# Optimization experiments

Measured on AMD Instinct MI355X. Metric: run time of the kernel, lower is better.

The kernel has to match this reference:

```python
import jax, jax.numpy as jnp
import numpy as np

B, S, D_IN = 4, 2048, 1024
H, D_HEAD = 16, 64  # num_head, num_out; H*D_HEAD == D_IN here
LN_EPS = 1e-5


def setup_inputs() -> dict:
    key = jax.random.key(0)
    ks = jax.random.split(key, 5)
    scale = 1.0 / np.sqrt(D_IN)
    return {
        "x": jax.random.normal(ks[0], (B, S, D_IN), dtype=jnp.float32),
        "Wq": jax.random.normal(ks[1], (H * D_HEAD, D_IN), dtype=jnp.float32) * scale,
        "Wk": jax.random.normal(ks[2], (H * D_HEAD, D_IN), dtype=jnp.float32) * scale,
        "Wv": jax.random.normal(ks[3], (H * D_HEAD, D_IN), dtype=jnp.float32) * scale,
        "Wr": jax.random.normal(ks[4], (H * D_HEAD, D_IN), dtype=jnp.float32) * scale,
        "gamma": jnp.ones((H * D_HEAD,), dtype=jnp.float32),
        "beta": jnp.zeros((H * D_HEAD,), dtype=jnp.float32),
    }


def reference(x, Wq, Wk, Wv, Wr, gamma, beta):
    b, s, _ = x.shape
    # Linear (no bias), torch weight layout [out, in]; split heads head-major
    q = (x @ Wq.T).reshape(b, s, H, D_HEAD)
    k = (x @ Wk.T).reshape(b, s, H, D_HEAD)
    v = (x @ Wv.T).reshape(b, s, H, D_HEAD)
    # full O(S^2) score matrix, as in the original
    scores = jnp.einsum("bqhd,bkhd->bhqk", q, k) / jnp.sqrt(jnp.float32(D_HEAD))
    weights = jax.nn.softmax(scores, axis=-1)
    attn = jnp.einsum("bhqk,bkhd->bqhd", weights, v).reshape(b, s, H * D_HEAD)
    out = jax.nn.relu(attn + x @ Wr.T)
    # LayerNorm over last dim with affine params
    mu = jnp.mean(out, axis=-1, keepdims=True)
    var = jnp.mean(jnp.square(out - mu), axis=-1, keepdims=True)
    out = (out - mu) * jax.lax.rsqrt(var + LN_EPS) * gamma + beta
    return out
```

## Files before the change

kernel.cpp:

```cpp
#include <hip/hip_runtime.h>
#include <hip/hip_bf16.h>
#include <stdint.h>

constexpr int BB = 4;
constexpr int SS = 2048;
constexpr int DIN = 1024;
constexpr int HH = 16;
constexpr int DH = 64;
constexpr int NOUT = 4096;
constexpr int MROWS = BB * SS;

typedef __attribute__((ext_vector_type(8))) short bf16x8;
typedef __attribute__((ext_vector_type(8))) unsigned short u16x8;
typedef __attribute__((ext_vector_type(4))) unsigned short u16x4;
typedef __attribute__((ext_vector_type(4))) float f32x4;

__device__ __forceinline__ unsigned short f2bf(float f) {
  unsigned int x = __float_as_uint(f);
  unsigned int r = (x + 0x7fffu + ((x >> 16) & 1u)) >> 16;
  return (unsigned short)r;
}
__device__ __forceinline__ float bf2f(unsigned short u) {
  return __uint_as_float(((unsigned int)u) << 16);
}

__device__ __forceinline__ void gload16(const void* g, void* l) {
  typedef __attribute__((address_space(1))) void gvoid;
  typedef __attribute__((address_space(3))) void lvoid;
  __builtin_amdgcn_global_load_lds((gvoid*)(uintptr_t)g, (lvoid*)l, 16, 0, 0);
}

__global__ __launch_bounds__(256) void convert_x(const float* __restrict__ src,
                                                 unsigned short* __restrict__ dst) {
  int i = (blockIdx.x * 256 + threadIdx.x) * 8;
  f32x4 a = *(const f32x4*)(src + i);
  f32x4 b = *(const f32x4*)(src + i + 4);
  u16x8 o;
  o[0] = f2bf(a[0]); o[1] = f2bf(a[1]); o[2] = f2bf(a[2]); o[3] = f2bf(a[3]);
  o[4] = f2bf(b[0]); o[5] = f2bf(b[1]); o[6] = f2bf(b[2]); o[7] = f2bf(b[3]);
  *(u16x8*)(dst + i) = o;
}

__global__ __launch_bounds__(256) void convert_w(const float* __restrict__ Wq,
                                                 const float* __restrict__ Wk,
                                                 const float* __restrict__ Wv,
                                                 const float* __restrict__ Wr,
                                                 unsigned short* __restrict__ dst) {
  int i = (blockIdx.x * 256 + threadIdx.x) * 8;
  int seg = i >> 20;
  const float* src = (seg == 0) ? Wq : (seg == 1) ? Wk : (seg == 2) ? Wv : Wr;
  float scale = (seg == 0) ? 0.125f * 1.44269504088896f : 1.0f;
  int j = i & 1048575;
  f32x4 a = *(const f32x4*)(src + j);
  f32x4 b = *(const f32x4*)(src + j + 4);
  u16x8 o;
  o[0] = f2bf(a[0] * scale); o[1] = f2bf(a[1] * scale);
  o[2] = f2bf(a[2] * scale); o[3] = f2bf(a[3] * scale);
  o[4] = f2bf(b[0] * scale); o[5] = f2bf(b[1] * scale);
  o[6] = f2bf(b[2] * scale); o[7] = f2bf(b[3] * scale);
  *(u16x8*)(dst + i) = o;
}

constexpr int Bb_M = 128, Bb_N = 128, Bb_K = 32;

__global__ __launch_bounds__(256) void gemm_qkvr(const unsigned short* __restrict__ X,
                                                 const unsigned short* __restrict__ Wt,
                                                 unsigned short* __restrict__ Y) {
  const int K = DIN;
  const int nbn = NOUT / Bb_N;
  int bid = blockIdx.x;
  int idx = (bid & 7) * 256 + (bid >> 3);
  int bm = idx / nbn, bn = idx % nbn;
  int m0 = bm * Bb_M, n0 = bn * Bb_N;
  int t = threadIdx.x;
  int w = t >> 6, l = t & 63;
  int lg = l >> 4, ll = l & 15;
  int wm = (w >> 1) * 64, wn = (w & 1) * 64;

  __shared__ unsigned short As[Bb_M * Bb_K];
  __shared__ unsigned short Bs[Bb_N * Bb_K];

  f32x4 acc[4][4];
#pragma unroll
  for (int i = 0; i < 4; i++)
#pragma unroll
    for (int j = 0; j < 4; j++) acc[i][j] = (f32x4)0.0f;

  for (int k0 = 0; k0 < K; k0 += Bb_K) {
    __syncthreads();
#pragma unroll
    for (int it = 0; it < 2; ++it) {
      int c = w * 2 + it;
      int row = c * 16 + (l >> 2);
      int col = (l & 3) * 8;
      gload16(X + (size_t)(m0 + row) * K + k0 + col, &As[c * 512]);
      gload16(Wt + (size_t)(n0 + row) * K + k0 + col, &Bs[c * 512]);
    }
    __syncthreads();
    bf16x8 a[4], b[4];
#pragma unroll
    for (int mt = 0; mt < 4; ++mt)
      a[mt] = *(const bf16x8*)&As[(wm + mt * 16 + ll) * Bb_K + lg * 8];
#pragma unroll
    for (int nt = 0; nt < 4; ++nt)
      b[nt] = *(const bf16x8*)&Bs[(wn + nt * 16 + ll) * Bb_K + lg * 8];
#pragma unroll
    for (int mt = 0; mt < 4; ++mt)
#pragma unroll
      for (int nt = 0; nt < 4; ++nt)
        acc[mt][nt] = __builtin_amdgcn_mfma_f32_16x16x32_bf16(a[mt], b[nt], acc[mt][nt], 0, 0, 0);
  }
#pragma unroll
  for (int mt = 0; mt < 4; ++mt)
#pragma unroll
    for (int nt = 0; nt < 4; ++nt) {
      int n = n0 + wn + nt * 16 + ll;
#pragma unroll
      for (int r = 0; r < 4; ++r) {
        int m = m0 + wm + mt * 16 + lg * 4 + r;
        Y[(size_t)m * NOUT + n] = f2bf(acc[mt][nt][r]);
      }
    }
}

__global__ __launch_bounds__(256) void transpose_v(const unsigned short* __restrict__ qkvr,
                                                   unsigned short* __restrict__ vt) {
  int bh = blockIdx.x >> 5;
  int st = blockIdx.x & 31;
  int b = bh >> 4, h = bh & 15;
  __shared__ unsigned short tile[64][72];
  int t = threadIdx.x;
#pragma unroll
  for (int c = 0; c < 2; ++c) {
    int chunk = t + c * 256;
    int row = chunk >> 3;
    int col = (chunk & 7) * 8;
    u16x8 v = *(const u16x8*)(qkvr + (size_t)(b * SS + st * 64 + row) * NOUT + 2048 + h * DH + col);
    *(u16x8*)&tile[row][col] = v;
  }
  __syncthreads();
  int d = t >> 2;
  int s0 = (t & 3) * 16;
  u16x8 o0, o1;
#pragma unroll
  for (int i = 0; i < 8; ++i) o0[i] = tile[s0 + i][d];
#pragma unroll
  for (int i = 0; i < 8; ++i) o1[i] = tile[s0 + 8 + i][d];
  size_t orow = (size_t)(bh * DH + d) * SS + st * 64 + s0;
  *(u16x8*)(vt + orow) = o0;
  *(u16x8*)(vt + orow + 8) = o1;
}

__global__ __launch_bounds__(512) void attention(const unsigned short* __restrict__ qkvr,
                                                 const unsigned short* __restrict__ vt,
                                                 unsigned short* __restrict__ attn) {
  int bid = blockIdx.x;
  int idx = (bid & 7) * 64 + (bid >> 3);
  int qt = idx & 7;
  int bh = idx >> 3;
  int b = bh >> 4, h = bh & 15;
  int t = threadIdx.x, w = t >> 6, l = t & 63;
  int lg = l >> 4, ll = l & 15;

  __shared__ unsigned short Ks[2][4096];
  __shared__ unsigned short Vs[2][4096];
  __shared__ unsigned short Ps[8][2048];

  const unsigned short* kbase = qkvr + (size_t)(b * SS) * NOUT + 1024 + h * DH;
  const unsigned short* vbase = vt + (size_t)(bh * DH) * SS;

  bf16x8 qb[2][2];
#pragma unroll
  for (int m = 0; m < 2; ++m) {
    int qrow = b * SS + qt * 256 + w * 32 + m * 16 + ll;
#pragma unroll
    for (int kk = 0; kk < 2; ++kk)
      qb[m][kk] = *(const bf16x8*)(qkvr + (size_t)qrow * NOUT + h * DH + kk * 32 + lg * 8);
  }

  f32x4 acc[2][4];
#pragma unroll
  for (int m = 0; m < 2; ++m)
#pragma unroll
    for (int i = 0; i < 4; i++) acc[m][i] = (f32x4)0.0f;
  float lsum[2] = {0.0f, 0.0f};

  int grow = t >> 3;
  int gcol = ((t & 7) ^ (grow & 7)) * 8;

  auto stage = [&](int tile, int bi) {
    gload16(kbase + (size_t)(tile * 64 + grow) * NOUT + gcol, &Ks[bi][w * 512]);
    gload16(vbase + (size_t)grow * SS + tile * 64 + gcol, &Vs[bi][w * 512]);
  };

  stage(0, 0);

  for (int kt = 0; kt < 32; ++kt) {
    int bi = kt & 1;
    stage((kt + 1) & 31, bi ^ 1);
    asm volatile("s_waitcnt vmcnt(2)" ::: "memory");
    __builtin_amdgcn_s_barrier();
    __builtin_amdgcn_sched_barrier(0);

    f32x4 s[2][4];
#pragma unroll
    for (int m = 0; m < 2; ++m)
#pragma unroll
      for (int nt = 0; nt < 4; nt++) s[m][nt] = (f32x4)0.0f;
    __builtin_amdgcn_s_setprio(1);
#pragma unroll
    for (int nt = 0; nt < 4; ++nt)
#pragma unroll
      for (int kk = 0; kk < 2; ++kk) {
        bf16x8 kb = *(const bf16x8*)&Ks[bi][(nt * 16 + ll) * 64 + ((kk * 4 + lg) ^ (ll & 7)) * 8];
        s[0][nt] = __builtin_amdgcn_mfma_f32_16x16x32_bf16(kb, qb[0][kk], s[0][nt], 0, 0, 0);
        s[1][nt] = __builtin_amdgcn_mfma_f32_16x16x32_bf16(kb, qb[1][kk], s[1][nt], 0, 0, 0);
      }
    __builtin_amdgcn_s_setprio(0);

#pragma unroll
    for (int m = 0; m < 2; ++m) {
      float ps = 0.0f;
#pragma unroll
      for (int nt = 0; nt < 4; nt++)
#pragma unroll
        for (int r = 0; r < 4; r++) {
          float e;
          asm("v_exp_f32 %0, %1" : "=v"(e) : "v"(s[m][nt][r]));
          s[m][nt][r] = e;
          ps += e;
        }
      lsum[m] += ps;
    }

#pragma unroll
    for (int m = 0; m < 2; ++m) {
      char* prow = (char*)&Ps[w][0] + (m * 16 + ll) * 128;
#pragma unroll
      for (int nt = 0; nt < 4; nt++) {
        unsigned sp0, sp1;
        asm("v_cvt_pk_bf16_f32 %0, %1, %2" : "=v"(sp0) : "v"(s[m][nt][0]), "v"(s[m][nt][1]));
        asm("v_cvt_pk_bf16_f32 %0, %1, %2" : "=v"(sp1) : "v"(s[m][nt][2]), "v"(s[m][nt][3]));
        uint2 pv; pv.x = sp0; pv.y = sp1;
        *(uint2*)(prow + ((2 * nt + (lg >> 1)) ^ (ll & 7)) * 16 + (lg & 1) * 8) = pv;
      }
    }

    bf16x8 pa[2][2];
#pragma unroll
    for (int m = 0; m < 2; ++m)
#pragma unroll
      for (int kk = 0; kk < 2; ++kk)
        pa[m][kk] = *(const bf16x8*)((char*)&Ps[w][0] + (m * 16 + ll) * 128 +
                                     ((4 * kk + lg) ^ (ll & 7)) * 16);

    __builtin_amdgcn_s_setprio(1);
#pragma unroll
    for (int kk = 0; kk < 2; ++kk) {
#pragma unroll
      for (int dt = 0; dt < 4; ++dt) {
        bf16x8 vb = *(const bf16x8*)&Vs[bi][(dt * 16 + ll) * 64 + ((kk * 4 + lg) ^ (ll & 7)) * 8];
        acc[0][dt] = __builtin_amdgcn_mfma_f32_16x16x32_bf16(pa[0][kk], vb, acc[0][dt], 0, 0, 0);
        acc[1][dt] = __builtin_amdgcn_mfma_f32_16x16x32_bf16(pa[1][kk], vb, acc[1][dt], 0, 0, 0);
      }
    }
    __builtin_amdgcn_s_setprio(0);
    __builtin_amdgcn_s_barrier();
    __builtin_amdgcn_sched_barrier(0);
  }
  asm volatile("s_waitcnt vmcnt(0)" ::: "memory");

  float inv[2][4];
#pragma unroll
  for (int m = 0; m < 2; ++m) {
    float lr = lsum[m];
    lr += __shfl_xor(lr, 16);
    lr += __shfl_xor(lr, 32);
#pragma unroll
    for (int r = 0; r < 4; r++)
      inv[m][r] = 1.0f / __shfl(lr, lg * 4 + r);
  }
#pragma unroll
  for (int m = 0; m < 2; ++m)
#pragma unroll
    for (int r = 0; r < 4; r++) {
      int arow = b * SS + qt * 256 + w * 32 + m * 16 + lg * 4 + r;
#pragma unroll
      for (int dt = 0; dt < 4; dt++)
        attn[(size_t)arow * DIN + h * DH + dt * 16 + ll] = f2bf(acc[m][dt][r] * inv[m][r]);
    }
}

__global__ __launch_bounds__(256) void ln_epilogue(const unsigned short* __restrict__ attn,
                                                   const unsigned short* __restrict__ qkvr,
                                                   const float* __restrict__ gamma,
                                                   const float* __restrict__ beta,
                                                   float* __restrict__ out) {
  int row = blockIdx.x;
  int t = threadIdx.x;
  u16x4 av = *(const u16x4*)(attn + (size_t)row * DIN + t * 4);
  u16x4 rv = *(const u16x4*)(qkvr + (size_t)row * NOUT + 3072 + t * 4);
  float v[4];
  float s = 0.0f, s2 = 0.0f;
#pragma unroll
  for (int i = 0; i < 4; i++) {
    v[i] = fmaxf(bf2f(av[i]) + bf2f(rv[i]), 0.0f);
    s += v[i];
    s2 += v[i] * v[i];
  }
#pragma unroll
  for (int m = 1; m < 64; m <<= 1) {
    s += __shfl_xor(s, m);
    s2 += __shfl_xor(s2, m);
  }
  __shared__ float red[2][4];
  int w = t >> 6, l = t & 63;
  if (l == 0) { red[0][w] = s; red[1][w] = s2; }
  __syncthreads();
  s = red[0][0] + red[0][1] + red[0][2] + red[0][3];
  s2 = red[1][0] + red[1][1] + red[1][2] + red[1][3];
  float mu = s * (1.0f / 1024.0f);
  float var = s2 * (1.0f / 1024.0f) - mu * mu;
  float rstd = rsqrtf(var + 1e-5f);
  f32x4 g = *(const f32x4*)(gamma + t * 4);
  f32x4 be = *(const f32x4*)(beta + t * 4);
  f32x4 o;
#pragma unroll
  for (int i = 0; i < 4; i++) o[i] = (v[i] - mu) * rstd * g[i] + be[i];
  *(f32x4*)(out + (size_t)row * DIN + t * 4) = o;
}

extern "C" void kernel_launch(void* const* d_in, const int* in_sizes, int n_in,
                              void* d_out, int out_size, void* d_ws, size_t ws_size,
                              hipStream_t stream) {
  const float* x = (const float*)d_in[0];
  const float* Wq = (const float*)d_in[1];
  const float* Wk = (const float*)d_in[2];
  const float* Wv = (const float*)d_in[3];
  const float* Wr = (const float*)d_in[4];
  const float* gamma = (const float*)d_in[5];
  const float* beta = (const float*)d_in[6];
  float* out = (float*)d_out;

  char* ws = (char*)d_ws;
  unsigned short* x_bf = (unsigned short*)ws;
  unsigned short* w_bf = (unsigned short*)(ws + (16ull << 20));
  unsigned short* qkvr = (unsigned short*)(ws + (24ull << 20));
  unsigned short* vt   = (unsigned short*)(ws + (88ull << 20));
  unsigned short* attn = (unsigned short*)(ws + (104ull << 20));

  convert_x<<<4096, 256, 0, stream>>>(x, x_bf);
  convert_w<<<2048, 256, 0, stream>>>(Wq, Wk, Wv, Wr, w_bf);
  gemm_qkvr<<<(MROWS / Bb_M) * (NOUT / Bb_N), 256, 0, stream>>>(x_bf, w_bf, qkvr);
  transpose_v<<<2048, 256, 0, stream>>>(qkvr, vt);
  attention<<<512, 512, 0, stream>>>(qkvr, vt, attn);
  ln_epilogue<<<MROWS, 256, 0, stream>>>(attn, qkvr, gamma, beta, out);
}
```

Baseline: 196.4 us.

## Double-buffer QKVR GEMM with async LDS loads, XOR swizzle and BK=64

Rewrites the projection GEMM main loop to use two LDS buffers, each with a K-tile of 64. The loop prefetches the tile two steps ahead while MFMAs run on the current tile, and synchronises with explicit waitcnt and barriers instead of two __syncthreads per step. An XOR swizzle on the column slot is meant to cut LDS bank conflicts on fragment reads. LDS use grows to 64KB per block, which may limit occupancy. The wrapped prefetch on the final iterations issues redundant loads.

```diff
diff --git a/kernel.cpp b/kernel.cpp
--- a/kernel.cpp
+++ b/kernel.cpp
@@ -61,24 +61,24 @@
   *(u16x8*)(dst + i) = o;
 }
 
-constexpr int Bb_M = 128, Bb_N = 128, Bb_K = 32;
+constexpr int GBM = 128, GBN = 128, GBK = 64;
 
 __global__ __launch_bounds__(256) void gemm_qkvr(const unsigned short* __restrict__ X,
                                                  const unsigned short* __restrict__ Wt,
                                                  unsigned short* __restrict__ Y) {
   const int K = DIN;
-  const int nbn = NOUT / Bb_N;
+  const int nbn = NOUT / GBN;
   int bid = blockIdx.x;
   int idx = (bid & 7) * 256 + (bid >> 3);
   int bm = idx / nbn, bn = idx % nbn;
-  int m0 = bm * Bb_M, n0 = bn * Bb_N;
+  int m0 = bm * GBM, n0 = bn * GBN;
   int t = threadIdx.x;
   int w = t >> 6, l = t & 63;
   int lg = l >> 4, ll = l & 15;
   int wm = (w >> 1) * 64, wn = (w & 1) * 64;
 
-  __shared__ unsigned short As[Bb_M * Bb_K];
-  __shared__ unsigned short Bs[Bb_N * Bb_K];
+  __shared__ unsigned short As[2][GBM * GBK];
+  __shared__ unsigned short Bs[2][GBN * GBK];
 
   f32x4 acc[4][4];
 #pragma unroll
@@ -86,30 +86,64 @@
 #pragma unroll
     for (int j = 0; j < 4; j++) acc[i][j] = (f32x4)0.0f;
 
-  for (int k0 = 0; k0 < K; k0 += Bb_K) {
-    __syncthreads();
-#pragma unroll
-    for (int it = 0; it < 2; ++it) {
-      int c = w * 2 + it;
-      int row = c * 16 + (l >> 2);
-      int col = (l & 3) * 8;
-      gload16(X + (size_t)(m0 + row) * K + k0 + col, &As[c * 512]);
-      gload16(Wt + (size_t)(n0 + row) * K + k0 + col, &Bs[c * 512]);
-    }
-    __syncthreads();
-    bf16x8 a[4], b[4];
+  int grow = t >> 3;
+  int gslot = t & 7;
+
+  auto stage = [&](int kt, int bi) {
+    int k0 = kt * GBK;
+#pragma unroll
+    for (int c = 0; c < 4; ++c) {
+      int row = c * 32 + grow;
+      int col = (gslot ^ (row & 7)) * 8;
+      gload16(X + (size_t)(m0 + row) * K + k0 + col, &As[bi][c * 2048 + w * 512]);
+      gload16(Wt + (size_t)(n0 + row) * K + k0 + col, &Bs[bi][c * 2048 + w * 512]);
+    }
+  };
+
+  stage(0, 0);
+  stage(1, 1);
+  asm volatile("s_waitcnt vmcnt(8)" ::: "memory");
+  __builtin_amdgcn_s_barrier();
+  __builtin_amdgcn_sched_barrier(0);
+
+  for (int kt = 0; kt < 16; ++kt) {
+    int cur = kt & 1;
+    bf16x8 af[4][2], bfr[4][2];
 #pragma unroll
     for (int mt = 0; mt < 4; ++mt)
-      a[mt] = *(const bf16x8*)&As[(wm + mt * 16 + ll) * Bb_K + lg * 8];
+#pragma unroll
+      for (int kk = 0; kk < 2; ++kk)
+        af[mt][kk] = *(const bf16x8*)&As[cur][(wm + mt * 16 + ll) * GBK +
+                                             ((kk * 4 + lg) ^ (ll & 7)) * 8];
 #pragma unroll
     for (int nt = 0; nt < 4; ++nt)
-      b[nt] = *(const bf16x8*)&Bs[(wn + nt * 16 + ll) * Bb_K + lg * 8];
+#pragma unroll
+      for (int kk = 0; kk < 2; ++kk)
+        bfr[nt][kk] = *(const bf16x8*)&Bs[cur][(wn + nt * 16 + ll) * GBK +
+                                              ((kk * 4 + lg) ^ (ll & 7)) * 8];
+    asm volatile("s_waitcnt lgkmcnt(0)" ::: "memory");
+    __builtin_amdgcn_s_barrier();
+    __builtin_amdgcn_sched_barrier(0);
+
+    stage((kt + 2) & 15, cur);
+
+    __builtin_amdgcn_s_setprio(1);
 #pragma unroll
     for (int mt = 0; mt < 4; ++mt)
 #pragma unroll
       for (int nt = 0; nt < 4; ++nt)
-        acc[mt][nt] = __builtin_amdgcn_mfma_f32_16x16x32_bf16(a[mt], b[nt], acc[mt][nt], 0, 0, 0);
-  }
+#pragma unroll
+        for (int kk = 0; kk < 2; ++kk)
+          acc[mt][nt] = __builtin_amdgcn_mfma_f32_16x16x32_bf16(af[mt][kk], bfr[nt][kk],
+                                                                acc[mt][nt], 0, 0, 0);
+    __builtin_amdgcn_s_setprio(0);
+
+    asm volatile("s_waitcnt vmcnt(8)" ::: "memory");
+    __builtin_amdgcn_s_barrier();
+    __builtin_amdgcn_sched_barrier(0);
+  }
+  asm volatile("s_waitcnt vmcnt(0)" ::: "memory");
+
 #pragma unroll
   for (int mt = 0; mt < 4; ++mt)
 #pragma unroll
@@ -351,7 +385,7 @@
 
   convert_x<<<4096, 256, 0, stream>>>(x, x_bf);
   convert_w<<<2048, 256, 0, stream>>>(Wq, Wk, Wv, Wr, w_bf);
-  gemm_qkvr<<<(MROWS / Bb_M) * (NOUT / Bb_N), 256, 0, stream>>>(x_bf, w_bf, qkvr);
+  gemm_qkvr<<<(MROWS / GBM) * (NOUT / GBN), 256, 0, stream>>>(x_bf, w_bf, qkvr);
   transpose_v<<<2048, 256, 0, stream>>>(qkvr, vt);
   attention<<<512, 512, 0, stream>>>(qkvr, vt, attn);
   ln_epilogue<<<MROWS, 256, 0, stream>>>(attn, qkvr, gamma, beta, out);
```

Measured after the change: 199.4 us. Within noise of the previous version (+1.5%).
